# Kernel optimization log

Hardware: AMD Instinct MI355X
Metric: run time of the kernel (lower is better)

## Reference

```python
import jax, jax.numpy as jnp
import numpy as np

B, TE, TD, D = 8, 2048, 2048, 256

def setup_inputs() -> dict:
    key = jax.random.key(0)
    k1, k2 = jax.random.split(key)
    encoder_outputs = jax.random.normal(k1, (B, TE, D), dtype=jnp.float32)
    decoder_outputs = jax.random.normal(k2, (B, TD, D), dtype=jnp.float32)
    return {"encoder_outputs": encoder_outputs, "decoder_outputs": decoder_outputs}

def reference(encoder_outputs, decoder_outputs):
    # luong_score[b,e,t] = sum_d enc[b,e,d] * dec[b,t,d]   (batch_dot with dec transposed)
    luong_score = jnp.einsum('bed,btd->bet', encoder_outputs, decoder_outputs)
    # softmax over encoder-time axis (axis=1)
    luong_score = jax.nn.softmax(luong_score, axis=1)
    # original does expand_dims + broadcast-multiply + sum over axis=1;
    # same math as a contraction over e: context[b,t,d] = sum_e score[b,e,t]*enc[b,e,d]
    encoder_vector = jnp.einsum('bet,bed->btd', luong_score, encoder_outputs)
    return jnp.concatenate([decoder_outputs, encoder_vector], axis=-1)
```

## Files before the change

### kernel.cpp

```cpp
#include <hip/hip_runtime.h>

typedef _Float16 f16;
typedef _Float16 f16x2 __attribute__((ext_vector_type(2)));
typedef _Float16 f16x4 __attribute__((ext_vector_type(4)));
typedef _Float16 f16x8 __attribute__((ext_vector_type(8)));
typedef float    f32x4 __attribute__((ext_vector_type(4)));

#define NB   8
#define TE   2048
#define TD   2048
#define DIM  256
#define NBTD (NB * TD)
#define LOG2E 1.44269504088896340736f

#define AS1(p) ((const __attribute__((address_space(1))) void*)(p))
#define AS3(p) ((__attribute__((address_space(3))) void*)(p))
#define MFMA16(a,b,c) __builtin_amdgcn_mfma_f32_16x16x32_f16((a),(b),(c),0,0,0)
#define SHUF8(x,y) __builtin_shufflevector((x),(y),0,1,2,3,4,5,6,7)

__device__ __forceinline__ unsigned lds_u32(void* p) {
    return (unsigned)(size_t)((__attribute__((address_space(3))) void*)p);
}
__device__ __forceinline__ f16x4 tr_rd0(unsigned a) {
    f16x4 r;
    asm volatile("ds_read_b64_tr_b16 %0, %1" : "=v"(r) : "v"(a));
    return r;
}
__device__ __forceinline__ f16x4 tr_rd1(unsigned a) {
    f16x4 r;
    asm volatile("ds_read_b64_tr_b16 %0, %1 offset:2048" : "=v"(r) : "v"(a));
    return r;
}

__global__ __launch_bounds__(256) void prep_kernel(const float* __restrict__ enc,
                                                   f16* __restrict__ ench) {
    size_t i = ((size_t)blockIdx.x * 256 + threadIdx.x) * 8;
    float4 v0 = *(const float4*)(enc + i);
    float4 v1 = *(const float4*)(enc + i + 4);
    f16x8 o;
    o[0]=(f16)v0.x; o[1]=(f16)v0.y; o[2]=(f16)v0.z; o[3]=(f16)v0.w;
    o[4]=(f16)v1.x; o[5]=(f16)v1.y; o[6]=(f16)v1.z; o[7]=(f16)v1.w;
    *(f16x8*)(ench + i) = o;
}

__global__ __launch_bounds__(256, 3) void attn_kernel(
        const float* __restrict__ dec32,
        const f16*  __restrict__ enc_h,
        f16*   __restrict__ ctxp,
        f16x2* __restrict__ ml,
        float* __restrict__ out) {
    __shared__ __align__(16) char lds[37888];
    const int tid  = threadIdx.x;
    const int lane = tid & 63;
    const int wv   = tid >> 6;
    const int tcol = lane & 15;
    const int q    = lane >> 4;

    const int x  = blockIdx.x;
    const int b  = x & 7;
    const int xb = (x >> 3) | (blockIdx.y << 2);
    const int z  = blockIdx.z;
    const int t0 = xb * 64 + wv * 16;
    const int tile0 = (64 * z) / 3;
    const int iters = (64 * (z + 1)) / 3 - tile0;

    const char* encb = (const char*)(enc_h + (size_t)b * TE * DIM);

    const int c0  = wv * 64 + lane;
    const int e_l = ((c0 >> 7) << 2) | ((c0 >> 1) & 3);
    const int d_l = (((c0 >> 3) & 15) << 4) | ((c0 & 1) << 3);
    const int stage_goff = e_l * (DIM * 2) + d_l * 2;
    char* stage_dst = lds + wv * 1024;

    const int qk_b0 = (tcol >> 2) * 2048 + (q >> 1) * 128 + (tcol & 3) * 32 + (q & 1) * 16;
    const int qk_b1 = qk_b0 + 8192;
    const unsigned tr_base = (unsigned)(q * 4096 + tcol * 8);
    const unsigned lds_base = lds_u32(lds);
    char* pb = lds + 32768 + wv * 1280;

    f16x8 qf[8];
    {
        const float* qrow = dec32 + ((size_t)b * TD + t0 + tcol) * DIM + q * 8;
        #pragma unroll
        for (int ks = 0; ks < 8; ks++) {
            float4 u = *(const float4*)(qrow + ks * 32);
            float4 v = *(const float4*)(qrow + ks * 32 + 4);
            f16x8 o;
            o[0]=(f16)u.x; o[1]=(f16)u.y; o[2]=(f16)u.z; o[3]=(f16)u.w;
            o[4]=(f16)v.x; o[5]=(f16)v.y; o[6]=(f16)v.z; o[7]=(f16)v.w;
            qf[ks] = o;
        }
    }

    {
        const char* s = encb + (size_t)tile0 * 16384 + stage_goff;
        #pragma unroll
        for (int i = 0; i < 4; i++)
            __builtin_amdgcn_global_load_lds(AS1(s + i * 4096), AS3(stage_dst + i * 4096), 16, 0, 0);
    }

    const f32x4 zero4 = {0.f, 0.f, 0.f, 0.f};
    float m_ = -INFINITY, l_ = 0.f;
    f32x4 ctx[16];
    #pragma unroll
    for (int dm = 0; dm < 16; dm++) ctx[dm] = zero4;

    __syncthreads();

    for (int it = 0; it < iters; ++it) {
        const int nat = (it & 1) << 14;
        if (it + 1 < iters) {
            const char* s = encb + (size_t)(tile0 + it + 1) * 16384 + stage_goff;
            char* dd = lds + (((it + 1) & 1) << 14) + wv * 1024;
            #pragma unroll
            for (int i = 0; i < 4; i++)
                __builtin_amdgcn_global_load_lds(AS1(s + i * 4096), AS3(dd + i * 4096), 16, 0, 0);
        }
        f32x4 st0 = zero4, st1 = zero4;
        const char* natp = lds + nat;
        #pragma unroll
        for (int ks = 0; ks < 8; ks++) {
            f16x8 af0 = *(const f16x8*)(natp + qk_b0 + ks * 256);
            f16x8 af1 = *(const f16x8*)(natp + qk_b1 + ks * 256);
            st0 = MFMA16(af0, qf[ks], st0);
            st1 = MFMA16(af1, qf[ks], st1);
        }
        float mx = fmaxf(fmaxf(fmaxf(st0[0], st0[1]), fmaxf(st0[2], st0[3])),
                         fmaxf(fmaxf(st1[0], st1[1]), fmaxf(st1[2], st1[3])));
        mx = fmaxf(mx, __shfl_xor(mx, 16, 64));
        mx = fmaxf(mx, __shfl_xor(mx, 32, 64));
        float ms = (float)(f16)fmaxf(m_, mx);
        float al = __builtin_amdgcn_exp2f((m_ - ms) * LOG2E);
        bool bump = ms > m_;
        m_ = ms;
        f16x4 pv0, pv1;
        float ssum = 0.f;
        #pragma unroll
        for (int r = 0; r < 4; r++) {
            float p0 = __builtin_amdgcn_exp2f((st0[r] - ms) * LOG2E);
            float p1 = __builtin_amdgcn_exp2f((st1[r] - ms) * LOG2E);
            pv0[r] = (f16)p0; pv1[r] = (f16)p1;
            ssum += (float)pv0[r] + (float)pv1[r];
        }
        *(f16x4*)(pb + tcol * 80 + q * 8)      = pv0;
        *(f16x4*)(pb + tcol * 80 + 32 + q * 8) = pv1;
        ssum += __shfl_xor(ssum, 16, 64);
        ssum += __shfl_xor(ssum, 32, 64);
        l_ = l_ * al + ssum;
        if (__any(bump)) {
            #pragma unroll
            for (int dm = 0; dm < 16; dm++) {
                ctx[dm][0] *= al; ctx[dm][1] *= al;
                ctx[dm][2] *= al; ctx[dm][3] *= al;
            }
        }
        f16x8 pf = *(const f16x8*)(pb + tcol * 80 + q * 16);
        const unsigned trb = lds_base + (unsigned)nat + tr_base;
        #pragma unroll
        for (int bb = 0; bb < 4; bb++) {
            const unsigned ab = trb + (unsigned)(bb * 512);
            f16x4 a0 = tr_rd0(ab);        f16x4 a1 = tr_rd1(ab);
            f16x4 a2 = tr_rd0(ab + 128);  f16x4 a3 = tr_rd1(ab + 128);
            f16x4 a4 = tr_rd0(ab + 256);  f16x4 a5 = tr_rd1(ab + 256);
            f16x4 a6 = tr_rd0(ab + 384);  f16x4 a7 = tr_rd1(ab + 384);
            asm volatile("s_waitcnt lgkmcnt(0)" ::: "memory");
            __builtin_amdgcn_sched_barrier(0);
            ctx[bb * 4 + 0] = MFMA16(SHUF8(a0, a1), pf, ctx[bb * 4 + 0]);
            ctx[bb * 4 + 1] = MFMA16(SHUF8(a2, a3), pf, ctx[bb * 4 + 1]);
            ctx[bb * 4 + 2] = MFMA16(SHUF8(a4, a5), pf, ctx[bb * 4 + 2]);
            ctx[bb * 4 + 3] = MFMA16(SHUF8(a6, a7), pf, ctx[bb * 4 + 3]);
        }
        __syncthreads();
    }

    const float inv = 1.0f / l_;
    const size_t row = (size_t)b * TD + t0 + tcol;
    if (z == 0) {
        f16* cb = ctxp + row * DIM;
        #pragma unroll
        for (int dm = 0; dm < 16; dm++) {
            f16x4 cv;
            #pragma unroll
            for (int r = 0; r < 4; r++) cv[r] = (f16)(ctx[dm][r] * inv);
            *(f16x4*)(cb + dm * 16 + q * 4) = cv;
        }
    } else {
        float* ob = out + row * 512 + (z == 2 ? 256 : 0);
        #pragma unroll
        for (int dm = 0; dm < 16; dm++) {
            float4 cv;
            cv.x = ctx[dm][0] * inv; cv.y = ctx[dm][1] * inv;
            cv.z = ctx[dm][2] * inv; cv.w = ctx[dm][3] * inv;
            *(float4*)(ob + dm * 16 + q * 4) = cv;
        }
    }
    if (q == 0) {
        f16x2 v; v[0] = (f16)m_; v[1] = (f16)l_;
        ml[(size_t)z * NBTD + row] = v;
    }
}

__global__ __launch_bounds__(256) void combine_kernel(const float* __restrict__ dec32,
        const f16* __restrict__ ctxp, const f16x2* __restrict__ ml,
        float* __restrict__ out) {
    int idx  = blockIdx.x * 256 + threadIdx.x;
    int trow = idx >> 5;
    int dg   = (idx & 31) * 8;
    float m0[3], l0[3], M = -INFINITY;
    #pragma unroll
    for (int s = 0; s < 3; s++) {
        f16x2 v = ml[(size_t)s * NBTD + trow];
        m0[s] = (float)v[0];
        l0[s] = (float)v[1];
        M = fmaxf(M, m0[s]);
    }
    float L = 0.f, w[3];
    #pragma unroll
    for (int s = 0; s < 3; s++) {
        w[s] = __builtin_amdgcn_exp2f((m0[s] - M) * LOG2E) * l0[s];
        L += w[s];
    }
    float invL = 1.0f / L;
    float acc[8];
    {
        f16x8 v = *(const f16x8*)(ctxp + (size_t)trow * DIM + dg);
        float w0 = w[0] * invL;
        #pragma unroll
        for (int j = 0; j < 8; j++) acc[j] = w0 * (float)v[j];
    }
    {
        const float* o1 = out + (size_t)trow * 512 + dg;
        float4 p0 = *(const float4*)(o1);
        float4 p1 = *(const float4*)(o1 + 4);
        float w1 = w[1] * invL;
        acc[0] += w1 * p0.x; acc[1] += w1 * p0.y; acc[2] += w1 * p0.z; acc[3] += w1 * p0.w;
        acc[4] += w1 * p1.x; acc[5] += w1 * p1.y; acc[6] += w1 * p1.z; acc[7] += w1 * p1.w;
    }
    {
        const float* o2 = out + (size_t)trow * 512 + 256 + dg;
        float4 p0 = *(const float4*)(o2);
        float4 p1 = *(const float4*)(o2 + 4);
        float w2 = w[2] * invL;
        acc[0] += w2 * p0.x; acc[1] += w2 * p0.y; acc[2] += w2 * p0.z; acc[3] += w2 * p0.w;
        acc[4] += w2 * p1.x; acc[5] += w2 * p1.y; acc[6] += w2 * p1.z; acc[7] += w2 * p1.w;
    }
    float4 d0 = *(const float4*)(dec32 + (size_t)trow * DIM + dg);
    float4 d1 = *(const float4*)(dec32 + (size_t)trow * DIM + dg + 4);
    float* ob = out + (size_t)trow * 512;
    *(float4*)(ob + dg)     = d0;
    *(float4*)(ob + dg + 4) = d1;
    float4 c0, c1;
    c0.x=acc[0]; c0.y=acc[1]; c0.z=acc[2]; c0.w=acc[3];
    c1.x=acc[4]; c1.y=acc[5]; c1.z=acc[6]; c1.w=acc[7];
    *(float4*)(ob + 256 + dg)     = c0;
    *(float4*)(ob + 256 + dg + 4) = c1;
}

extern "C" void kernel_launch(void* const* d_in, const int* in_sizes, int n_in,
                              void* d_out, int out_size, void* d_ws, size_t ws_size,
                              hipStream_t stream) {
    (void)in_sizes; (void)n_in;
    const float* enc = (const float*)d_in[0];
    const float* dec = (const float*)d_in[1];
    float* out = (float*)d_out;

    const size_t MLB = (size_t)3 * NBTD * 4;
    const size_t HB  = (size_t)NB * TE * DIM * 2;
    const size_t CSL = (size_t)NBTD * DIM * 2;
    const size_t NEED = MLB + HB + CSL;

    if (ws_size < NEED) {
        hipMemsetAsync(d_out, 0, (size_t)out_size * sizeof(float), stream);
        return;
    }
    f16x2* ml   = (f16x2*)d_ws;
    f16*   ench = (f16*)((char*)d_ws + MLB);
    f16*   ctxp = (f16*)((char*)d_ws + MLB + HB);

    prep_kernel<<<2048, 256, 0, stream>>>(enc, ench);
    attn_kernel<<<dim3(32, 8, 3), 256, 0, stream>>>(dec, ench, ctxp, ml, out);
    combine_kernel<<<2048, 256, 0, stream>>>(dec, ctxp, ml, out);
}
```

Before: 148.8 us.

## Restructure attention tiles: 32 queries per block, waves split over encoder and D

Reorganizes the attention kernel so each block handles 32 decoder rows. The four waves split the 64-row encoder tile for QK and split the output D dimension for PV. Per-wave row maxima and sums are exchanged through LDS, and the P tile is swizzled to avoid bank conflicts. The encoder split drops from three to two chunks of 1024 rows, so the combine kernel merges two partials instead of three. The aim is to reuse each staged encoder tile across more queries and to cut partial-result traffic, at the cost of extra block barriers per iteration, larger LDS use and lower occupancy (2 blocks per CU).

```diff
diff --git a/kernel.cpp b/kernel.cpp
--- a/kernel.cpp
+++ b/kernel.cpp
@@ -21,16 +21,8 @@
 __device__ __forceinline__ unsigned lds_u32(void* p) {
     return (unsigned)(size_t)((__attribute__((address_space(3))) void*)p);
 }
-__device__ __forceinline__ f16x4 tr_rd0(unsigned a) {
-    f16x4 r;
-    asm volatile("ds_read_b64_tr_b16 %0, %1" : "=v"(r) : "v"(a));
-    return r;
-}
-__device__ __forceinline__ f16x4 tr_rd1(unsigned a) {
-    f16x4 r;
-    asm volatile("ds_read_b64_tr_b16 %0, %1 offset:2048" : "=v"(r) : "v"(a));
-    return r;
-}
+#define TR_RD(dst, a, OFFS) \
+    asm volatile("ds_read_b64_tr_b16 %0, %1 offset:" OFFS : "=v"(dst) : "v"(a))
 
 __global__ __launch_bounds__(256) void prep_kernel(const float* __restrict__ enc,
                                                    f16* __restrict__ ench) {
@@ -43,160 +35,216 @@
     *(f16x8*)(ench + i) = o;
 }
 
-__global__ __launch_bounds__(256, 3) void attn_kernel(
+#define NATSZ  32768
+#define LDS_P  65536
+#define LDS_X  69632
+
+__global__ __launch_bounds__(256, 2) void attn_kernel(
         const float* __restrict__ dec32,
         const f16*  __restrict__ enc_h,
         f16*   __restrict__ ctxp,
         f16x2* __restrict__ ml,
         float* __restrict__ out) {
-    __shared__ __align__(16) char lds[37888];
+    __shared__ __align__(16) char lds[70144];
     const int tid  = threadIdx.x;
     const int lane = tid & 63;
-    const int wv   = tid >> 6;
+    const int w    = tid >> 6;
     const int tcol = lane & 15;
     const int q    = lane >> 4;
 
-    const int x  = blockIdx.x;
-    const int b  = x & 7;
-    const int xb = (x >> 3) | (blockIdx.y << 2);
+    const int b  = blockIdx.x;
+    const int t0 = blockIdx.y * 32;
     const int z  = blockIdx.z;
-    const int t0 = xb * 64 + wv * 16;
-    const int tile0 = (64 * z) / 3;
-    const int iters = (64 * (z + 1)) / 3 - tile0;
+    const int tile0 = z * 16;
+    const int ITERS = 16;
 
     const char* encb = (const char*)(enc_h + (size_t)b * TE * DIM);
 
-    const int c0  = wv * 64 + lane;
-    const int e_l = ((c0 >> 7) << 2) | ((c0 >> 1) & 3);
-    const int d_l = (((c0 >> 3) & 15) << 4) | ((c0 & 1) << 3);
-    const int stage_goff = e_l * (DIM * 2) + d_l * 2;
-    char* stage_dst = lds + wv * 1024;
-
-    const int qk_b0 = (tcol >> 2) * 2048 + (q >> 1) * 128 + (tcol & 3) * 32 + (q & 1) * 16;
-    const int qk_b1 = qk_b0 + 8192;
-    const unsigned tr_base = (unsigned)(q * 4096 + tcol * 8);
-    const unsigned lds_base = lds_u32(lds);
-    char* pb = lds + 32768 + wv * 1280;
-
-    f16x8 qf[8];
+    const int e0s = ((tid >> 7) << 2) | ((tid >> 1) & 3);
+    const int dss = (((tid >> 3) & 15) << 4) | ((tid & 1) << 3);
+    const int sgo = e0s * 512 + dss * 2;
+    char* sdst = lds + tid * 16;
+
+    const int qkb = (4 * w + (tcol >> 2)) * 2048 + (q >> 1) * 128
+                  + (tcol & 3) * 32 + (q & 1) * 16;
+    const int pwo  = LDS_P + tcol * 128 + (((w * 2 + (q >> 1)) ^ (tcol & 7)) << 4)
+                   + ((q & 1) << 3);
+    const int pf0o = LDS_P + tcol * 128 + ((q ^ (tcol & 3)) << 4)
+                   + (((tcol >> 2) & 1) << 6);
+    const int pf1o = pf0o ^ 64;
+    const unsigned TRB = lds_u32(lds) + (unsigned)(q * 4096 + w * 512 + tcol * 8);
+
+    f16x8 qf[2][8];
     {
         const float* qrow = dec32 + ((size_t)b * TD + t0 + tcol) * DIM + q * 8;
         #pragma unroll
+        for (int tn = 0; tn < 2; tn++)
+            #pragma unroll
+            for (int ks = 0; ks < 8; ks++) {
+                const float* p = qrow + (size_t)tn * 16 * DIM + ks * 32;
+                float4 u0 = *(const float4*)(p);
+                float4 v0 = *(const float4*)(p + 4);
+                f16x8 o;
+                o[0]=(f16)u0.x; o[1]=(f16)u0.y; o[2]=(f16)u0.z; o[3]=(f16)u0.w;
+                o[4]=(f16)v0.x; o[5]=(f16)v0.y; o[6]=(f16)v0.z; o[7]=(f16)v0.w;
+                qf[tn][ks] = o;
+            }
+    }
+
+    {
+        const char* s = encb + (size_t)tile0 * 32768 + sgo;
+        #pragma unroll
+        for (int i = 0; i < 8; i++)
+            __builtin_amdgcn_global_load_lds(AS1(s + i * 4096), AS3(sdst + i * 4096), 16, 0, 0);
+    }
+
+    const f32x4 zero4 = {0.f, 0.f, 0.f, 0.f};
+    float m_[2] = {-INFINITY, -INFINITY};
+    float l_[2] = {0.f, 0.f};
+    f32x4 ctx[4][2];
+    #pragma unroll
+    for (int dd = 0; dd < 4; dd++) { ctx[dd][0] = zero4; ctx[dd][1] = zero4; }
+
+    __syncthreads();
+
+    for (int it = 0; it < ITERS; ++it) {
+        const int nat = (it & 1) << 15;
+        f32x4 st[2] = {zero4, zero4};
+        const char* natp = lds + nat + qkb;
+        #pragma unroll
         for (int ks = 0; ks < 8; ks++) {
-            float4 u = *(const float4*)(qrow + ks * 32);
-            float4 v = *(const float4*)(qrow + ks * 32 + 4);
-            f16x8 o;
-            o[0]=(f16)u.x; o[1]=(f16)u.y; o[2]=(f16)u.z; o[3]=(f16)u.w;
-            o[4]=(f16)v.x; o[5]=(f16)v.y; o[6]=(f16)v.z; o[7]=(f16)v.w;
-            qf[ks] = o;
-        }
-    }
-
-    {
-        const char* s = encb + (size_t)tile0 * 16384 + stage_goff;
-        #pragma unroll
-        for (int i = 0; i < 4; i++)
-            __builtin_amdgcn_global_load_lds(AS1(s + i * 4096), AS3(stage_dst + i * 4096), 16, 0, 0);
-    }
-
-    const f32x4 zero4 = {0.f, 0.f, 0.f, 0.f};
-    float m_ = -INFINITY, l_ = 0.f;
-    f32x4 ctx[16];
-    #pragma unroll
-    for (int dm = 0; dm < 16; dm++) ctx[dm] = zero4;
-
-    __syncthreads();
-
-    for (int it = 0; it < iters; ++it) {
-        const int nat = (it & 1) << 14;
-        if (it + 1 < iters) {
-            const char* s = encb + (size_t)(tile0 + it + 1) * 16384 + stage_goff;
-            char* dd = lds + (((it + 1) & 1) << 14) + wv * 1024;
-            #pragma unroll
-            for (int i = 0; i < 4; i++)
-                __builtin_amdgcn_global_load_lds(AS1(s + i * 4096), AS3(dd + i * 4096), 16, 0, 0);
-        }
-        f32x4 st0 = zero4, st1 = zero4;
-        const char* natp = lds + nat;
-        #pragma unroll
-        for (int ks = 0; ks < 8; ks++) {
-            f16x8 af0 = *(const f16x8*)(natp + qk_b0 + ks * 256);
-            f16x8 af1 = *(const f16x8*)(natp + qk_b1 + ks * 256);
-            st0 = MFMA16(af0, qf[ks], st0);
-            st1 = MFMA16(af1, qf[ks], st1);
-        }
-        float mx = fmaxf(fmaxf(fmaxf(st0[0], st0[1]), fmaxf(st0[2], st0[3])),
-                         fmaxf(fmaxf(st1[0], st1[1]), fmaxf(st1[2], st1[3])));
-        mx = fmaxf(mx, __shfl_xor(mx, 16, 64));
-        mx = fmaxf(mx, __shfl_xor(mx, 32, 64));
-        float ms = (float)(f16)fmaxf(m_, mx);
-        float al = __builtin_amdgcn_exp2f((m_ - ms) * LOG2E);
-        bool bump = ms > m_;
-        m_ = ms;
-        f16x4 pv0, pv1;
-        float ssum = 0.f;
-        #pragma unroll
-        for (int r = 0; r < 4; r++) {
-            float p0 = __builtin_amdgcn_exp2f((st0[r] - ms) * LOG2E);
-            float p1 = __builtin_amdgcn_exp2f((st1[r] - ms) * LOG2E);
-            pv0[r] = (f16)p0; pv1[r] = (f16)p1;
-            ssum += (float)pv0[r] + (float)pv1[r];
-        }
-        *(f16x4*)(pb + tcol * 80 + q * 8)      = pv0;
-        *(f16x4*)(pb + tcol * 80 + 32 + q * 8) = pv1;
-        ssum += __shfl_xor(ssum, 16, 64);
-        ssum += __shfl_xor(ssum, 32, 64);
-        l_ = l_ * al + ssum;
+            f16x8 af = *(const f16x8*)(natp + ks * 256);
+            st[0] = MFMA16(af, qf[0][ks], st[0]);
+            st[1] = MFMA16(af, qf[1][ks], st[1]);
+        }
+        #pragma unroll
+        for (int tn = 0; tn < 2; tn++) {
+            float m0 = fmaxf(fmaxf(st[tn][0], st[tn][1]), fmaxf(st[tn][2], st[tn][3]));
+            m0 = fmaxf(m0, __shfl_xor(m0, 16, 64));
+            m0 = fmaxf(m0, __shfl_xor(m0, 32, 64));
+            if (q == 0) *(float*)(lds + LDS_X + (tn * 16 + tcol) * 16 + w * 4) = m0;
+        }
+        __syncthreads();
+        if (it + 1 < ITERS) {
+            const char* s = encb + (size_t)(tile0 + it + 1) * 32768 + sgo;
+            char* dd2 = lds + (((it + 1) & 1) << 15) + tid * 16;
+            #pragma unroll
+            for (int i = 0; i < 8; i++)
+                __builtin_amdgcn_global_load_lds(AS1(s + i * 4096), AS3(dd2 + i * 4096), 16, 0, 0);
+        }
+        bool bump = false;
+        float al[2];
+        #pragma unroll
+        for (int tn = 0; tn < 2; tn++) {
+            float4 m4 = *(const float4*)(lds + LDS_X + (tn * 16 + tcol) * 16);
+            float mm = fmaxf(fmaxf(m4.x, m4.y), fmaxf(m4.z, m4.w));
+            float ms = (float)(f16)fmaxf(m_[tn], mm);
+            al[tn] = __builtin_amdgcn_exp2f((m_[tn] - ms) * LOG2E);
+            bump = bump || (ms > m_[tn]);
+            m_[tn] = ms;
+            f16x4 pv;
+            float ssum = 0.f;
+            #pragma unroll
+            for (int r = 0; r < 4; r++) {
+                float p = __builtin_amdgcn_exp2f((st[tn][r] - ms) * LOG2E);
+                pv[r] = (f16)p;
+                ssum += (float)pv[r];
+            }
+            *(f16x4*)(lds + pwo + tn * 2048) = pv;
+            ssum += __shfl_xor(ssum, 16, 64);
+            ssum += __shfl_xor(ssum, 32, 64);
+            l_[tn] = l_[tn] * al[tn] + ssum;
+        }
         if (__any(bump)) {
             #pragma unroll
-            for (int dm = 0; dm < 16; dm++) {
-                ctx[dm][0] *= al; ctx[dm][1] *= al;
-                ctx[dm][2] *= al; ctx[dm][3] *= al;
-            }
-        }
-        f16x8 pf = *(const f16x8*)(pb + tcol * 80 + q * 16);
-        const unsigned trb = lds_base + (unsigned)nat + tr_base;
-        #pragma unroll
-        for (int bb = 0; bb < 4; bb++) {
-            const unsigned ab = trb + (unsigned)(bb * 512);
-            f16x4 a0 = tr_rd0(ab);        f16x4 a1 = tr_rd1(ab);
-            f16x4 a2 = tr_rd0(ab + 128);  f16x4 a3 = tr_rd1(ab + 128);
-            f16x4 a4 = tr_rd0(ab + 256);  f16x4 a5 = tr_rd1(ab + 256);
-            f16x4 a6 = tr_rd0(ab + 384);  f16x4 a7 = tr_rd1(ab + 384);
+            for (int dd = 0; dd < 4; dd++)
+                #pragma unroll
+                for (int tn = 0; tn < 2; tn++) {
+                    ctx[dd][tn][0] *= al[tn]; ctx[dd][tn][1] *= al[tn];
+                    ctx[dd][tn][2] *= al[tn]; ctx[dd][tn][3] *= al[tn];
+                }
+        }
+        __syncthreads();
+        const unsigned trv = TRB + (unsigned)nat;
+        {
+            f16x8 pfA = *(const f16x8*)(lds + pf0o);
+            f16x8 pfB = *(const f16x8*)(lds + pf0o + 2048);
+            f16x4 t00,t01,t10,t11,t20,t21,t30,t31;
+            TR_RD(t00, trv, "0");    TR_RD(t01, trv, "2048");
+            TR_RD(t10, trv, "128");  TR_RD(t11, trv, "2176");
+            TR_RD(t20, trv, "256");  TR_RD(t21, trv, "2304");
+            TR_RD(t30, trv, "384");  TR_RD(t31, trv, "2432");
             asm volatile("s_waitcnt lgkmcnt(0)" ::: "memory");
             __builtin_amdgcn_sched_barrier(0);
-            ctx[bb * 4 + 0] = MFMA16(SHUF8(a0, a1), pf, ctx[bb * 4 + 0]);
-            ctx[bb * 4 + 1] = MFMA16(SHUF8(a2, a3), pf, ctx[bb * 4 + 1]);
-            ctx[bb * 4 + 2] = MFMA16(SHUF8(a4, a5), pf, ctx[bb * 4 + 2]);
-            ctx[bb * 4 + 3] = MFMA16(SHUF8(a6, a7), pf, ctx[bb * 4 + 3]);
+            f16x8 a0 = SHUF8(t00,t01), a1 = SHUF8(t10,t11);
+            f16x8 a2 = SHUF8(t20,t21), a3 = SHUF8(t30,t31);
+            ctx[0][0] = MFMA16(a0, pfA, ctx[0][0]); ctx[0][1] = MFMA16(a0, pfB, ctx[0][1]);
+            ctx[1][0] = MFMA16(a1, pfA, ctx[1][0]); ctx[1][1] = MFMA16(a1, pfB, ctx[1][1]);
+            ctx[2][0] = MFMA16(a2, pfA, ctx[2][0]); ctx[2][1] = MFMA16(a2, pfB, ctx[2][1]);
+            ctx[3][0] = MFMA16(a3, pfA, ctx[3][0]); ctx[3][1] = MFMA16(a3, pfB, ctx[3][1]);
+        }
+        {
+            f16x8 pfA = *(const f16x8*)(lds + pf1o);
+            f16x8 pfB = *(const f16x8*)(lds + pf1o + 2048);
+            f16x4 t00,t01,t10,t11,t20,t21,t30,t31;
+            TR_RD(t00, trv, "16384"); TR_RD(t01, trv, "18432");
+            TR_RD(t10, trv, "16512"); TR_RD(t11, trv, "18560");
+            TR_RD(t20, trv, "16640"); TR_RD(t21, trv, "18688");
+            TR_RD(t30, trv, "16768"); TR_RD(t31, trv, "18816");
+            asm volatile("s_waitcnt lgkmcnt(0)" ::: "memory");
+            __builtin_amdgcn_sched_barrier(0);
+            f16x8 a0 = SHUF8(t00,t01), a1 = SHUF8(t10,t11);
+            f16x8 a2 = SHUF8(t20,t21), a3 = SHUF8(t30,t31);
+            ctx[0][0] = MFMA16(a0, pfA, ctx[0][0]); ctx[0][1] = MFMA16(a0, pfB, ctx[0][1]);
+            ctx[1][0] = MFMA16(a1, pfA, ctx[1][0]); ctx[1][1] = MFMA16(a1, pfB, ctx[1][1]);
+            ctx[2][0] = MFMA16(a2, pfA, ctx[2][0]); ctx[2][1] = MFMA16(a2, pfB, ctx[2][1]);
+            ctx[3][0] = MFMA16(a3, pfA, ctx[3][0]); ctx[3][1] = MFMA16(a3, pfB, ctx[3][1]);
         }
         __syncthreads();
     }
 
-    const float inv = 1.0f / l_;
+    if (q == 0) {
+        *(float*)(lds + LDS_X + tcol * 16 + w * 4)        = l_[0];
+        *(float*)(lds + LDS_X + (16 + tcol) * 16 + w * 4) = l_[1];
+    }
+    __syncthreads();
+    float L[2], inv[2];
+    #pragma unroll
+    for (int tn = 0; tn < 2; tn++) {
+        float4 l4 = *(const float4*)(lds + LDS_X + (tn * 16 + tcol) * 16);
+        L[tn]   = (l4.x + l4.y) + (l4.z + l4.w);
+        inv[tn] = 1.0f / L[tn];
+    }
     const size_t row = (size_t)b * TD + t0 + tcol;
     if (z == 0) {
-        f16* cb = ctxp + row * DIM;
-        #pragma unroll
-        for (int dm = 0; dm < 16; dm++) {
-            f16x4 cv;
-            #pragma unroll
-            for (int r = 0; r < 4; r++) cv[r] = (f16)(ctx[dm][r] * inv);
-            *(f16x4*)(cb + dm * 16 + q * 4) = cv;
-        }
+        f16* cb = ctxp + row * DIM + w * 64;
+        #pragma unroll
+        for (int tn = 0; tn < 2; tn++)
+            #pragma unroll
+            for (int dd = 0; dd < 4; dd++) {
+                f16x4 cv;
+                #pragma unroll
+                for (int r = 0; r < 4; r++) cv[r] = (f16)(ctx[dd][tn][r] * inv[tn]);
+                *(f16x4*)(cb + (size_t)tn * 16 * DIM + dd * 16 + q * 4) = cv;
+            }
     } else {
-        float* ob = out + row * 512 + (z == 2 ? 256 : 0);
-        #pragma unroll
-        for (int dm = 0; dm < 16; dm++) {
-            float4 cv;
-            cv.x = ctx[dm][0] * inv; cv.y = ctx[dm][1] * inv;
-            cv.z = ctx[dm][2] * inv; cv.w = ctx[dm][3] * inv;
-            *(float4*)(ob + dm * 16 + q * 4) = cv;
-        }
-    }
-    if (q == 0) {
-        f16x2 v; v[0] = (f16)m_; v[1] = (f16)l_;
-        ml[(size_t)z * NBTD + row] = v;
+        float* ob = out + row * 512 + 256 + w * 64;
+        #pragma unroll
+        for (int tn = 0; tn < 2; tn++)
+            #pragma unroll
+            for (int dd = 0; dd < 4; dd++) {
+                float4 cv;
+                cv.x = ctx[dd][tn][0] * inv[tn]; cv.y = ctx[dd][tn][1] * inv[tn];
+                cv.z = ctx[dd][tn][2] * inv[tn]; cv.w = ctx[dd][tn][3] * inv[tn];
+                *(float4*)(ob + (size_t)tn * 16 * 512 + dd * 16 + q * 4) = cv;
+            }
+    }
+    if (w == 0 && q == 0) {
+        #pragma unroll
+        for (int tn = 0; tn < 2; tn++) {
+            f16x2 v; v[0] = (f16)m_[tn]; v[1] = (f16)L[tn];
+            ml[(size_t)z * NBTD + row + tn * 16] = v;
+        }
     }
 }
 
@@ -206,43 +254,27 @@
     int idx  = blockIdx.x * 256 + threadIdx.x;
     int trow = idx >> 5;
     int dg   = (idx & 31) * 8;
-    float m0[3], l0[3], M = -INFINITY;
-    #pragma unroll
-    for (int s = 0; s < 3; s++) {
-        f16x2 v = ml[(size_t)s * NBTD + trow];
-        m0[s] = (float)v[0];
-        l0[s] = (float)v[1];
-        M = fmaxf(M, m0[s]);
-    }
-    float L = 0.f, w[3];
-    #pragma unroll
-    for (int s = 0; s < 3; s++) {
-        w[s] = __builtin_amdgcn_exp2f((m0[s] - M) * LOG2E) * l0[s];
-        L += w[s];
-    }
-    float invL = 1.0f / L;
+    f16x2 v0 = ml[trow];
+    f16x2 v1 = ml[(size_t)NBTD + trow];
+    float m0 = (float)v0[0], l0 = (float)v0[1];
+    float m1 = (float)v1[0], l1 = (float)v1[1];
+    float M  = fmaxf(m0, m1);
+    float w0 = __builtin_amdgcn_exp2f((m0 - M) * LOG2E) * l0;
+    float w1 = __builtin_amdgcn_exp2f((m1 - M) * LOG2E) * l1;
+    float invL = 1.0f / (w0 + w1);
+    w0 *= invL; w1 *= invL;
     float acc[8];
     {
         f16x8 v = *(const f16x8*)(ctxp + (size_t)trow * DIM + dg);
-        float w0 = w[0] * invL;
         #pragma unroll
         for (int j = 0; j < 8; j++) acc[j] = w0 * (float)v[j];
     }
     {
-        const float* o1 = out + (size_t)trow * 512 + dg;
+        const float* o1 = out + (size_t)trow * 512 + 256 + dg;
         float4 p0 = *(const float4*)(o1);
         float4 p1 = *(const float4*)(o1 + 4);
-        float w1 = w[1] * invL;
         acc[0] += w1 * p0.x; acc[1] += w1 * p0.y; acc[2] += w1 * p0.z; acc[3] += w1 * p0.w;
         acc[4] += w1 * p1.x; acc[5] += w1 * p1.y; acc[6] += w1 * p1.z; acc[7] += w1 * p1.w;
-    }
-    {
-        const float* o2 = out + (size_t)trow * 512 + 256 + dg;
-        float4 p0 = *(const float4*)(o2);
-        float4 p1 = *(const float4*)(o2 + 4);
-        float w2 = w[2] * invL;
-        acc[0] += w2 * p0.x; acc[1] += w2 * p0.y; acc[2] += w2 * p0.z; acc[3] += w2 * p0.w;
-        acc[4] += w2 * p1.x; acc[5] += w2 * p1.y; acc[6] += w2 * p1.z; acc[7] += w2 * p1.w;
     }
     float4 d0 = *(const float4*)(dec32 + (size_t)trow * DIM + dg);
     float4 d1 = *(const float4*)(dec32 + (size_t)trow * DIM + dg + 4);
@@ -264,7 +296,7 @@
     const float* dec = (const float*)d_in[1];
     float* out = (float*)d_out;
 
-    const size_t MLB = (size_t)3 * NBTD * 4;
+    const size_t MLB = (size_t)2 * NBTD * 4;
     const size_t HB  = (size_t)NB * TE * DIM * 2;
     const size_t CSL = (size_t)NBTD * DIM * 2;
     const size_t NEED = MLB + HB + CSL;
@@ -278,6 +310,6 @@
     f16*   ctxp = (f16*)((char*)d_ws + MLB + HB);
 
     prep_kernel<<<2048, 256, 0, stream>>>(enc, ench);
-    attn_kernel<<<dim3(32, 8, 3), 256, 0, stream>>>(dec, ench, ctxp, ml, out);
+    attn_kernel<<<dim3(8, 64, 2), 256, 0, stream>>>(dec, ench, ctxp, ml, out);
     combine_kernel<<<2048, 256, 0, stream>>>(dec, ctxp, ml, out);
 }
```

Result: slower. 167.5 us (+12.6%).
